# Kernel optimization log

Measured on AMD Instinct MI355X. Metric: run time of the kernel, lower is better.

## Reference

```python
import jax, jax.numpy as jnp
import numpy as np

HIDDEN_DIM = 4096
NUM_EXPERTS = 64
THRESHOLD = 0.8


def setup_inputs() -> dict:
    key = jax.random.key(0)
    kx, kw = jax.random.split(key)
    x = jax.random.normal(kx, (4, 4096, HIDDEN_DIM), dtype=jnp.float32)
    # gate weight init: normal(0, 0.1), bias zeros (as in nn.init calls)
    W = jax.random.normal(kw, (HIDDEN_DIM, NUM_EXPERTS), dtype=jnp.float32) * 0.1
    b = jnp.zeros((NUM_EXPERTS,), dtype=jnp.float32)
    return {"x": x, "W": W, "b": b}


def reference(x, W, b):
    # logits: [B, S, E]
    logits = jnp.einsum('bsh,he->bse', x, W) + b
    probs = jax.nn.softmax(logits, axis=-1)
    # descending sort over experts
    order = jnp.argsort(-probs, axis=-1)                        # [B,S,E] int
    sorted_probs = jnp.take_along_axis(probs, order, axis=-1)   # [B,S,E]
    cum = jnp.cumsum(sorted_probs, axis=-1)
    mask = cum >= THRESHOLD                                     # [B,S,E] bool
    k_values = jnp.argmax(mask.astype(jnp.float32), axis=-1) + 1
    never = ~jnp.any(mask, axis=-1)
    k_values = jnp.where(never, NUM_EXPERTS, k_values)          # [B,S] int
    # Vectorized mask-and-scatter replacing the per-token Python loop.
    # Padded to NUM_EXPERTS (static max_k) for jit compatibility; slots
    # beyond k get expert=-1, prob=0 exactly as the torch fill defaults.
    slot = jnp.arange(NUM_EXPERTS)                              # [E]
    sel = slot[None, None, :] < k_values[..., None]             # [B,S,E]
    selected_experts = jnp.where(sel, order, -1)
    selected_probs = jnp.where(sel, sorted_probs, 0.0)
    return selected_experts, selected_probs, k_values
```

## Files before the change

kernel.cpp:

```cpp
#include <hip/hip_runtime.h>
#include <math.h>

#define HID 4096
#define NEXP 64
#define NTOK 16384

typedef __attribute__((ext_vector_type(8))) short short8;
typedef __attribute__((ext_vector_type(8))) __bf16 bf16x8;
typedef __attribute__((ext_vector_type(4))) float f32x4;

__global__ __launch_bounds__(256) void wfrag_kernel(
    const float* __restrict__ W, short* __restrict__ wfh,
    short* __restrict__ wfl, unsigned int* __restrict__ flag_count) {
  if (blockIdx.x == 0 && threadIdx.x == 0) *flag_count = 0u;
  int gid = blockIdx.x * 256 + threadIdx.x;
  int l  = gid & 63;
  int nt = (gid >> 6) & 3;
  int ks = gid >> 8;
  int e  = nt * 16 + (l & 15);
  int k0 = ks * 32 + (l >> 4) * 8;
  bf16x8 h8, l8;
#pragma unroll
  for (int j = 0; j < 8; ++j) {
    float w = W[(size_t)(k0 + j) * NEXP + e];
    __bf16 h = (__bf16)w;
    h8[j] = h;
    l8[j] = (__bf16)(w - (float)h);
  }
  ((short8*)wfh)[gid] = __builtin_bit_cast(short8, h8);
  ((short8*)wfl)[gid] = __builtin_bit_cast(short8, l8);
}

template <int P>
__device__ __forceinline__ void issue_b(const short8*& wh, const short8*& wl,
                                        short8 (&rbh)[2][4],
                                        short8 (&rbl)[2][4]) {
#pragma unroll
  for (int nt = 0; nt < 4; ++nt) {
    rbh[P][nt] = wh[nt * 64];
    rbl[P][nt] = wl[nt * 64];
  }
  wh += 256;
  wl += 256;
}

template <int P>
__device__ __forceinline__ void issue_g(const float* (&xp)[4][2],
                                        float* wavebase ) {
#pragma unroll
  for (int st = 0; st < 4; ++st)
#pragma unroll
    for (int p = 0; p < 2; ++p)
      __builtin_amdgcn_global_load_lds(xp[st][p],
                                       wavebase + P * 2048 + st * 512 + p * 256,
                                       16, 0, 0);
#pragma unroll
  for (int st = 0; st < 4; ++st) {
    xp[st][0] += 32;
    xp[st][1] += 32;
  }
}

template <int P>
__device__ __forceinline__ void compute_c(const float* wavebase,
                                          short8 (&rbh)[2][4],
                                          short8 (&rbl)[2][4],
                                          f32x4 (&acc)[4][4], int l) {
  const int lr = l >> 4;
  const int s0 = ((2 * lr) ^ (l & 7)) * 16;
  const char* cb = (const char*)(wavebase + P * 2048);
#pragma unroll
  for (int st = 0; st < 4; ++st) {
    const char* rowbase =
        cb + st * 2048 + ((l >> 3) & 1) * 1024 + (l & 7) * 128;
    float4 lo = *(const float4*)(rowbase + s0);
    float4 hi = *(const float4*)(rowbase + (s0 ^ 16));
    float xv[8] = {lo.x, lo.y, lo.z, lo.w, hi.x, hi.y, hi.z, hi.w};
    bf16x8 ah, al;
#pragma unroll
    for (int j = 0; j < 8; ++j) {
      __bf16 h = (__bf16)xv[j];
      ah[j] = h;
      al[j] = (__bf16)(xv[j] - (float)h);
    }
#pragma unroll
    for (int nt = 0; nt < 4; ++nt) {
      bf16x8 vh = __builtin_bit_cast(bf16x8, rbh[P][nt]);
      bf16x8 vl = __builtin_bit_cast(bf16x8, rbl[P][nt]);
      acc[st][nt] = __builtin_amdgcn_mfma_f32_16x16x32_bf16(ah, vh, acc[st][nt], 0, 0, 0);
      acc[st][nt] = __builtin_amdgcn_mfma_f32_16x16x32_bf16(al, vh, acc[st][nt], 0, 0, 0);
      acc[st][nt] = __builtin_amdgcn_mfma_f32_16x16x32_bf16(ah, vl, acc[st][nt], 0, 0, 0);
      acc[st][nt] = __builtin_amdgcn_mfma_f32_16x16x32_bf16(al, vl, acc[st][nt], 0, 0, 0);
    }
  }
}

#define SB __builtin_amdgcn_sched_barrier(0)
#define WAIT16 asm volatile("s_waitcnt vmcnt(16)" ::: "memory")
#define WAIT0  asm volatile("s_waitcnt vmcnt(0)" ::: "memory")

__global__ __launch_bounds__(512, 2) void gemm_kernel(
    const float* __restrict__ x, const short* __restrict__ wfh,
    const short* __restrict__ wfl, float* __restrict__ partial) {
  __shared__ float smem[32768];

  const int t = threadIdx.x;
  const int w = t >> 6;
  const int l = t & 63;
  const int lr = l >> 4;
  const int m0 = blockIdx.x * 64;
  const int kq = w * (HID / 8);

  float* wavebase = smem + w * 4096;

  const float* xp[4][2];
#pragma unroll
  for (int st = 0; st < 4; ++st)
#pragma unroll
    for (int p = 0; p < 2; ++p) {
      int g = (l & 7) ^ (l >> 3);
      int row = m0 + st * 16 + 8 * p + (l >> 3);
      xp[st][p] = x + (size_t)row * HID + kq + g * 4;
    }

  const short8* wh = (const short8*)wfh + (size_t)(w * 16 * 4) * 64 + l;
  const short8* wl = (const short8*)wfl + (size_t)(w * 16 * 4) * 64 + l;

  f32x4 acc[4][4];
#pragma unroll
  for (int st = 0; st < 4; ++st)
#pragma unroll
    for (int nt = 0; nt < 4; ++nt) acc[st][nt] = (f32x4){0.f, 0.f, 0.f, 0.f};

  short8 rbh[2][4], rbl[2][4];

  issue_b<0>(wh, wl, rbh, rbl);
  SB;
  issue_g<0>(xp, wavebase);
  SB;

#pragma unroll 1
  for (int c2 = 0; c2 < 7; ++c2) {
    issue_b<1>(wh, wl, rbh, rbl);
    SB;
    issue_g<1>(xp, wavebase);
    SB;
    WAIT16;
    SB;
    compute_c<0>(wavebase, rbh, rbl, acc, l);

    issue_b<0>(wh, wl, rbh, rbl);
    SB;
    issue_g<0>(xp, wavebase);
    SB;
    WAIT16;
    SB;
    compute_c<1>(wavebase, rbh, rbl, acc, l);
  }
  issue_b<1>(wh, wl, rbh, rbl);
  SB;
  issue_g<1>(xp, wavebase);
  SB;
  WAIT16;
  SB;
  compute_c<0>(wavebase, rbh, rbl, acc, l);
  WAIT0;
  SB;
  compute_c<1>(wavebase, rbh, rbl, acc, l);

  __syncthreads();
  float* red = smem;
  if (w >= 4) {
#pragma unroll
    for (int st = 0; st < 4; ++st)
#pragma unroll
      for (int nt = 0; nt < 4; ++nt)
#pragma unroll
        for (int r = 0; r < 4; ++r)
          red[((w - 4) * 64 + st * 16 + lr * 4 + r) * 68 + nt * 16 +
              (l & 15)] = acc[st][nt][r];
  }
  __syncthreads();
  if (w < 4) {
#pragma unroll
    for (int st = 0; st < 4; ++st)
#pragma unroll
      for (int nt = 0; nt < 4; ++nt)
#pragma unroll
        for (int r = 0; r < 4; ++r) {
          int row = st * 16 + lr * 4 + r;
          float s = acc[st][nt][r] +
                    red[(w * 64 + row) * 68 + nt * 16 + (l & 15)];
          partial[((size_t)w * NTOK + m0 + row) * NEXP + nt * 16 + (l & 15)] =
              s;
        }
  }
}

__global__ __launch_bounds__(256) void route_kernel(
    const float* __restrict__ partial, const float* __restrict__ b,
    float* __restrict__ out_exp, float* __restrict__ out_prob,
    float* __restrict__ out_k, unsigned int* __restrict__ flag_count,
    int* __restrict__ flag_list) {
  const int tok = (int)((blockIdx.x * 256 + threadIdx.x) >> 6);
  const int l   = threadIdx.x & 63;

  float p0 = partial[((size_t)0 * NTOK + tok) * NEXP + l];
  float p1 = partial[((size_t)1 * NTOK + tok) * NEXP + l];
  float p2 = partial[((size_t)2 * NTOK + tok) * NEXP + l];
  float p3 = partial[((size_t)3 * NTOK + tok) * NEXP + l];
  float lgv = (p0 + p1) + (p2 + p3) + b[l];

  float mx = lgv;
#pragma unroll
  for (int off = 32; off; off >>= 1) mx = fmaxf(mx, __shfl_xor(mx, off));
  float ev = expf(lgv - mx);
  float sm = ev;
#pragma unroll
  for (int off = 32; off; off >>= 1) sm += __shfl_xor(sm, off);
  float p = ev / sm;

  float sp = p;
  int   si = l;
#pragma unroll
  for (int k = 2; k <= 64; k <<= 1) {
#pragma unroll
    for (int j = k >> 1; j > 0; j >>= 1) {
      float op = __shfl_xor(sp, j);
      int   oi = __shfl_xor(si, j);
      bool cmp  = (sp > op) || (sp == op && si < oi);
      bool keep = (cmp == (((l & k) == 0) == ((l & j) == 0)));
      if (!keep) { sp = op; si = oi; }
    }
  }

  float c = sp;
#pragma unroll
  for (int off = 1; off < 64; off <<= 1) {
    float tp = __shfl_up(c, off);
    if (l >= off) c += tp;
  }

  unsigned long long m = __ballot(c >= 0.8f);
  int kv = (m == 0ULL) ? NEXP : __ffsll(m);

  float spn = __shfl_down(sp, 1);
  bool pairRisk = (l < kv) && (l < 63) && ((sp - spn) < 1e-3f * (sp + spn));
  bool cumRisk  = fabsf(c - 0.8f) < 3e-4f;
  bool flagged  = (__ballot(pairRisk || cumRisk) != 0ULL);

  bool sel = l < kv;
  size_t base = (size_t)tok * NEXP;
  out_exp[base + l]  = sel ? (float)si : -1.0f;
  out_prob[base + l] = sel ? sp : 0.0f;
  if (l == 0) {
    out_k[tok] = (float)kv;
    if (flagged) {
      unsigned int idx = atomicAdd(flag_count, 1u);
      flag_list[idx] = tok;
    }
  }
}

__global__ __launch_bounds__(256) void router_repair(
    const float* __restrict__ x, const float* __restrict__ W,
    const float* __restrict__ b, const unsigned int* __restrict__ flag_count,
    const int* __restrict__ flag_list, float* __restrict__ out_exp,
    float* __restrict__ out_prob, float* __restrict__ out_k) {
  __shared__ double part[4][NEXP];
  const int t = threadIdx.x;
  const int e = t & 63;
  const int c = t >> 6;
  const int n = (int)*flag_count;

  for (int i = blockIdx.x; i < n; i += gridDim.x) {
    const int tok = flag_list[i];
    const float* xrow = x + (size_t)tok * HID;
    double s = 0.0;
    const int k0 = c * (HID / 4);
#pragma unroll 8
    for (int k = k0; k < k0 + HID / 4; ++k)
      s = fma((double)xrow[k], (double)W[(size_t)k * NEXP + e], s);
    part[c][e] = s;
    __syncthreads();

    if (t < 64) {
      double lgv = ((part[0][e] + part[1][e]) + part[2][e]) + part[3][e] +
                   (double)b[e];
      double mx = lgv;
#pragma unroll
      for (int off = 32; off; off >>= 1) mx = fmax(mx, __shfl_xor(mx, off));
      double ev = exp(lgv - mx);
      double sm = ev;
#pragma unroll
      for (int off = 32; off; off >>= 1) sm += __shfl_xor(sm, off);
      double p = ev / sm;

      double sp = p;
      int    si = e;
#pragma unroll
      for (int k = 2; k <= 64; k <<= 1) {
#pragma unroll
        for (int j = k >> 1; j > 0; j >>= 1) {
          double op = __shfl_xor(sp, j);
          int    oi = __shfl_xor(si, j);
          bool cmp  = (sp > op) || (sp == op && si < oi);
          bool keep = (cmp == (((e & k) == 0) == ((e & j) == 0)));
          if (!keep) { sp = op; si = oi; }
        }
      }

      double cc = sp;
#pragma unroll
      for (int off = 1; off < 64; off <<= 1) {
        double tp = __shfl_up(cc, off);
        if (e >= off) cc += tp;
      }

      unsigned long long m = __ballot(cc >= 0.8);
      int kv = (m == 0ULL) ? NEXP : __ffsll(m);

      bool sel = e < kv;
      size_t base = (size_t)tok * NEXP;
      out_exp[base + e]  = sel ? (float)si : -1.0f;
      out_prob[base + e] = sel ? (float)sp : 0.0f;
      if (e == 0) out_k[tok] = (float)kv;
    }
    __syncthreads();
  }
}

extern "C" void kernel_launch(void* const* d_in, const int* in_sizes, int n_in,
                              void* d_out, int out_size, void* d_ws,
                              size_t ws_size, hipStream_t stream) {
  const float* x = (const float*)d_in[0];
  const float* W = (const float*)d_in[1];
  const float* b = (const float*)d_in[2];

  float* out_exp  = (float*)d_out;
  float* out_prob = out_exp + (size_t)NTOK * NEXP;
  float* out_k    = out_prob + (size_t)NTOK * NEXP;

  short* wfh = (short*)d_ws;
  short* wfl = (short*)((char*)d_ws + (size_t)512 * 1024);
  unsigned int* flag_count = (unsigned int*)((char*)d_ws + (size_t)1024 * 1024);
  int* flag_list = (int*)((char*)d_ws + (size_t)1024 * 1024 + 256);
  float* partial = (float*)((char*)d_ws + (size_t)2 * 1024 * 1024);

  wfrag_kernel<<<128, 256, 0, stream>>>(W, wfh, wfl, flag_count);
  gemm_kernel<<<NTOK / 64, 512, 0, stream>>>(x, wfh, wfl, partial);
  route_kernel<<<NTOK * NEXP / 256, 256, 0, stream>>>(
      partial, b, out_exp, out_prob, out_k, flag_count, flag_list);
  router_repair<<<128, 256, 0, stream>>>(x, W, b, flag_count, flag_list,
                                         out_exp, out_prob, out_k);
}
```

Baseline: 117.4 us.

## Shrink GEMM token tile to 32 and write 8 split-K partial planes

The GEMM block now covers 32 tokens instead of 64 with smaller accumulators and a 2-stage LDS buffer, which allows 4 blocks per CU and doubles the grid. The in-block LDS reduction across wave pairs is removed, so each of 8 waves writes its own K-slice partial plane and the route kernel sums 8 planes instead of 4. This trades higher occupancy and less sync for twice as much partial-buffer traffic and twice as many W fragment reloads per token.

```diff
diff --git a/kernel.cpp b/kernel.cpp
--- a/kernel.cpp
+++ b/kernel.cpp
@@ -4,6 +4,7 @@
 #define HID 4096
 #define NEXP 64
 #define NTOK 16384
+#define NPLANE 8
 
 typedef __attribute__((ext_vector_type(8))) short short8;
 typedef __attribute__((ext_vector_type(8))) __bf16 bf16x8;
@@ -31,91 +32,25 @@
   ((short8*)wfl)[gid] = __builtin_bit_cast(short8, l8);
 }
 
-template <int P>
-__device__ __forceinline__ void issue_b(const short8*& wh, const short8*& wl,
-                                        short8 (&rbh)[2][4],
-                                        short8 (&rbl)[2][4]) {
-#pragma unroll
-  for (int nt = 0; nt < 4; ++nt) {
-    rbh[P][nt] = wh[nt * 64];
-    rbl[P][nt] = wl[nt * 64];
-  }
-  wh += 256;
-  wl += 256;
-}
-
-template <int P>
-__device__ __forceinline__ void issue_g(const float* (&xp)[4][2],
-                                        float* wavebase ) {
-#pragma unroll
-  for (int st = 0; st < 4; ++st)
-#pragma unroll
-    for (int p = 0; p < 2; ++p)
-      __builtin_amdgcn_global_load_lds(xp[st][p],
-                                       wavebase + P * 2048 + st * 512 + p * 256,
-                                       16, 0, 0);
-#pragma unroll
-  for (int st = 0; st < 4; ++st) {
-    xp[st][0] += 32;
-    xp[st][1] += 32;
-  }
-}
-
-template <int P>
-__device__ __forceinline__ void compute_c(const float* wavebase,
-                                          short8 (&rbh)[2][4],
-                                          short8 (&rbl)[2][4],
-                                          f32x4 (&acc)[4][4], int l) {
-  const int lr = l >> 4;
-  const int s0 = ((2 * lr) ^ (l & 7)) * 16;
-  const char* cb = (const char*)(wavebase + P * 2048);
-#pragma unroll
-  for (int st = 0; st < 4; ++st) {
-    const char* rowbase =
-        cb + st * 2048 + ((l >> 3) & 1) * 1024 + (l & 7) * 128;
-    float4 lo = *(const float4*)(rowbase + s0);
-    float4 hi = *(const float4*)(rowbase + (s0 ^ 16));
-    float xv[8] = {lo.x, lo.y, lo.z, lo.w, hi.x, hi.y, hi.z, hi.w};
-    bf16x8 ah, al;
-#pragma unroll
-    for (int j = 0; j < 8; ++j) {
-      __bf16 h = (__bf16)xv[j];
-      ah[j] = h;
-      al[j] = (__bf16)(xv[j] - (float)h);
-    }
-#pragma unroll
-    for (int nt = 0; nt < 4; ++nt) {
-      bf16x8 vh = __builtin_bit_cast(bf16x8, rbh[P][nt]);
-      bf16x8 vl = __builtin_bit_cast(bf16x8, rbl[P][nt]);
-      acc[st][nt] = __builtin_amdgcn_mfma_f32_16x16x32_bf16(ah, vh, acc[st][nt], 0, 0, 0);
-      acc[st][nt] = __builtin_amdgcn_mfma_f32_16x16x32_bf16(al, vh, acc[st][nt], 0, 0, 0);
-      acc[st][nt] = __builtin_amdgcn_mfma_f32_16x16x32_bf16(ah, vl, acc[st][nt], 0, 0, 0);
-      acc[st][nt] = __builtin_amdgcn_mfma_f32_16x16x32_bf16(al, vl, acc[st][nt], 0, 0, 0);
-    }
-  }
-}
-
 #define SB __builtin_amdgcn_sched_barrier(0)
-#define WAIT16 asm volatile("s_waitcnt vmcnt(16)" ::: "memory")
-#define WAIT0  asm volatile("s_waitcnt vmcnt(0)" ::: "memory")
-
-__global__ __launch_bounds__(512, 2) void gemm_kernel(
+#define WAIT4 asm volatile("s_waitcnt vmcnt(4)" ::: "memory")
+#define WAIT0 asm volatile("s_waitcnt vmcnt(0)" ::: "memory")
+
+__global__ __launch_bounds__(512, 4) void gemm_kernel(
     const float* __restrict__ x, const short* __restrict__ wfh,
     const short* __restrict__ wfl, float* __restrict__ partial) {
-  __shared__ float smem[32768];
+  __shared__ float xstage[8][2][1024];
 
   const int t = threadIdx.x;
   const int w = t >> 6;
   const int l = t & 63;
   const int lr = l >> 4;
-  const int m0 = blockIdx.x * 64;
+  const int m0 = blockIdx.x * 32;
   const int kq = w * (HID / 8);
 
-  float* wavebase = smem + w * 4096;
-
-  const float* xp[4][2];
-#pragma unroll
-  for (int st = 0; st < 4; ++st)
+  const float* xp[2][2];
+#pragma unroll
+  for (int st = 0; st < 2; ++st)
 #pragma unroll
     for (int p = 0; p < 2; ++p) {
       int g = (l & 7) ^ (l >> 3);
@@ -123,78 +58,103 @@
       xp[st][p] = x + (size_t)row * HID + kq + g * 4;
     }
 
-  const short8* wh = (const short8*)wfh + (size_t)(w * 16 * 4) * 64 + l;
-  const short8* wl = (const short8*)wfl + (size_t)(w * 16 * 4) * 64 + l;
-
-  f32x4 acc[4][4];
-#pragma unroll
-  for (int st = 0; st < 4; ++st)
+  const short8* wh = (const short8*)wfh + (size_t)(w * 16) * 256 + l;
+  const short8* wl = (const short8*)wfl + (size_t)(w * 16) * 256 + l;
+
+  f32x4 acc[2][4];
+#pragma unroll
+  for (int st = 0; st < 2; ++st)
 #pragma unroll
     for (int nt = 0; nt < 4; ++nt) acc[st][nt] = (f32x4){0.f, 0.f, 0.f, 0.f};
 
-  short8 rbh[2][4], rbl[2][4];
-
-  issue_b<0>(wh, wl, rbh, rbl);
+  short8 rbh[4], rbl[4];
+
+#pragma unroll
+  for (int st = 0; st < 2; ++st)
+#pragma unroll
+    for (int p = 0; p < 2; ++p)
+      __builtin_amdgcn_global_load_lds(xp[st][p],
+                                       &xstage[w][0][st * 512 + p * 256], 16,
+                                       0, 0);
   SB;
-  issue_g<0>(xp, wavebase);
+#pragma unroll
+  for (int nt = 0; nt < 4; ++nt) {
+    rbh[nt] = wh[nt * 64];
+    rbl[nt] = wl[nt * 64];
+  }
+  wh += 256;
+  wl += 256;
   SB;
 
 #pragma unroll 1
-  for (int c2 = 0; c2 < 7; ++c2) {
-    issue_b<1>(wh, wl, rbh, rbl);
+  for (int ch = 0; ch < 16; ++ch) {
+    const int cur = ch & 1;
+    if (ch < 15) {
+      const int nxt = cur ^ 1;
+#pragma unroll
+      for (int st = 0; st < 2; ++st)
+#pragma unroll
+        for (int p = 0; p < 2; ++p)
+          __builtin_amdgcn_global_load_lds(
+              xp[st][p] + (ch + 1) * 32,
+              &xstage[w][nxt][st * 512 + p * 256], 16, 0, 0);
+      SB;
+      WAIT4;
+    } else {
+      WAIT0;
+    }
     SB;
-    issue_g<1>(xp, wavebase);
+
+    {
+      const char* cb = (const char*)&xstage[w][cur][0];
+      const int s0 = ((2 * lr) ^ (l & 7)) * 16;
+#pragma unroll
+      for (int st = 0; st < 2; ++st) {
+        const char* rowbase =
+            cb + st * 2048 + ((l >> 3) & 1) * 1024 + (l & 7) * 128;
+        float4 lo = *(const float4*)(rowbase + s0);
+        float4 hi = *(const float4*)(rowbase + (s0 ^ 16));
+        float xv[8] = {lo.x, lo.y, lo.z, lo.w, hi.x, hi.y, hi.z, hi.w};
+        bf16x8 ah, al;
+#pragma unroll
+        for (int j = 0; j < 8; ++j) {
+          __bf16 h = (__bf16)xv[j];
+          ah[j] = h;
+          al[j] = (__bf16)(xv[j] - (float)h);
+        }
+#pragma unroll
+        for (int nt = 0; nt < 4; ++nt) {
+          bf16x8 vh = __builtin_bit_cast(bf16x8, rbh[nt]);
+          bf16x8 vl = __builtin_bit_cast(bf16x8, rbl[nt]);
+          acc[st][nt] = __builtin_amdgcn_mfma_f32_16x16x32_bf16(ah, vh, acc[st][nt], 0, 0, 0);
+          acc[st][nt] = __builtin_amdgcn_mfma_f32_16x16x32_bf16(al, vh, acc[st][nt], 0, 0, 0);
+          acc[st][nt] = __builtin_amdgcn_mfma_f32_16x16x32_bf16(ah, vl, acc[st][nt], 0, 0, 0);
+          acc[st][nt] = __builtin_amdgcn_mfma_f32_16x16x32_bf16(al, vl, acc[st][nt], 0, 0, 0);
+        }
+      }
+    }
     SB;
-    WAIT16;
+
+    if (ch < 15) {
+#pragma unroll
+      for (int nt = 0; nt < 4; ++nt) {
+        rbh[nt] = wh[nt * 64];
+        rbl[nt] = wl[nt * 64];
+      }
+      wh += 256;
+      wl += 256;
+    }
     SB;
-    compute_c<0>(wavebase, rbh, rbl, acc, l);
-
-    issue_b<0>(wh, wl, rbh, rbl);
-    SB;
-    issue_g<0>(xp, wavebase);
-    SB;
-    WAIT16;
-    SB;
-    compute_c<1>(wavebase, rbh, rbl, acc, l);
-  }
-  issue_b<1>(wh, wl, rbh, rbl);
-  SB;
-  issue_g<1>(xp, wavebase);
-  SB;
-  WAIT16;
-  SB;
-  compute_c<0>(wavebase, rbh, rbl, acc, l);
-  WAIT0;
-  SB;
-  compute_c<1>(wavebase, rbh, rbl, acc, l);
-
-  __syncthreads();
-  float* red = smem;
-  if (w >= 4) {
-#pragma unroll
-    for (int st = 0; st < 4; ++st)
-#pragma unroll
-      for (int nt = 0; nt < 4; ++nt)
-#pragma unroll
-        for (int r = 0; r < 4; ++r)
-          red[((w - 4) * 64 + st * 16 + lr * 4 + r) * 68 + nt * 16 +
-              (l & 15)] = acc[st][nt][r];
-  }
-  __syncthreads();
-  if (w < 4) {
-#pragma unroll
-    for (int st = 0; st < 4; ++st)
-#pragma unroll
-      for (int nt = 0; nt < 4; ++nt)
-#pragma unroll
-        for (int r = 0; r < 4; ++r) {
-          int row = st * 16 + lr * 4 + r;
-          float s = acc[st][nt][r] +
-                    red[(w * 64 + row) * 68 + nt * 16 + (l & 15)];
-          partial[((size_t)w * NTOK + m0 + row) * NEXP + nt * 16 + (l & 15)] =
-              s;
-        }
-  }
+  }
+
+#pragma unroll
+  for (int st = 0; st < 2; ++st)
+#pragma unroll
+    for (int nt = 0; nt < 4; ++nt)
+#pragma unroll
+      for (int r = 0; r < 4; ++r)
+        partial[((size_t)w * NTOK + m0 + st * 16 + lr * 4 + r) * NEXP +
+                nt * 16 + (l & 15)] = acc[st][nt][r];
 }
 
 __global__ __launch_bounds__(256) void route_kernel(
@@ -205,11 +165,12 @@
   const int tok = (int)((blockIdx.x * 256 + threadIdx.x) >> 6);
   const int l   = threadIdx.x & 63;
 
-  float p0 = partial[((size_t)0 * NTOK + tok) * NEXP + l];
-  float p1 = partial[((size_t)1 * NTOK + tok) * NEXP + l];
-  float p2 = partial[((size_t)2 * NTOK + tok) * NEXP + l];
-  float p3 = partial[((size_t)3 * NTOK + tok) * NEXP + l];
-  float lgv = (p0 + p1) + (p2 + p3) + b[l];
+  float p[NPLANE];
+#pragma unroll
+  for (int j = 0; j < NPLANE; ++j)
+    p[j] = partial[((size_t)j * NTOK + tok) * NEXP + l];
+  float lgv = (((p[0] + p[1]) + (p[2] + p[3])) +
+               ((p[4] + p[5]) + (p[6] + p[7]))) + b[l];
 
   float mx = lgv;
 #pragma unroll
@@ -218,9 +179,9 @@
   float sm = ev;
 #pragma unroll
   for (int off = 32; off; off >>= 1) sm += __shfl_xor(sm, off);
-  float p = ev / sm;
-
-  float sp = p;
+  float pr = ev / sm;
+
+  float sp = pr;
   int   si = l;
 #pragma unroll
   for (int k = 2; k <= 64; k <<= 1) {
@@ -348,7 +309,7 @@
   float* partial = (float*)((char*)d_ws + (size_t)2 * 1024 * 1024);
 
   wfrag_kernel<<<128, 256, 0, stream>>>(W, wfh, wfl, flag_count);
-  gemm_kernel<<<NTOK / 64, 512, 0, stream>>>(x, wfh, wfl, partial);
+  gemm_kernel<<<NTOK / 32, 512, 0, stream>>>(x, wfh, wfl, partial);
   route_kernel<<<NTOK * NEXP / 256, 256, 0, stream>>>(
       partial, b, out_exp, out_prob, out_k, flag_count, flag_list);
   router_repair<<<128, 256, 0, stream>>>(x, W, b, flag_count, flag_list,
```

After: 136.5 us. 1.16x slower.

## Fuse routing (softmax, sort, threshold) into GEMM epilogue via shared memory

Applied to the files above, without the earlier changes.

Merges the separate route kernel into the GEMM epilogue. All eight waves write their K-split partial accumulators to shared memory (odd stride to avoid bank conflicts), then each wave reduces and routes eight tokens. This removes the global partial-logits buffer round trip (4 x 16384 x 64 floats written and read back) and one kernel launch. The cost is a larger shared-memory footprint (about 130 KB per block), which may limit two blocks per CU. The routing epilogue is also now serialized inside the GEMM blocks.

```diff
diff --git a/kernel.cpp b/kernel.cpp
--- a/kernel.cpp
+++ b/kernel.cpp
@@ -4,6 +4,7 @@
 #define HID 4096
 #define NEXP 64
 #define NTOK 16384
+#define PSTR 65
 
 typedef __attribute__((ext_vector_type(8))) short short8;
 typedef __attribute__((ext_vector_type(8))) __bf16 bf16x8;
@@ -99,10 +100,13 @@
 #define WAIT16 asm volatile("s_waitcnt vmcnt(16)" ::: "memory")
 #define WAIT0  asm volatile("s_waitcnt vmcnt(0)" ::: "memory")
 
-__global__ __launch_bounds__(512, 2) void gemm_kernel(
+__global__ __launch_bounds__(512, 2) void gemm_route_kernel(
     const float* __restrict__ x, const short* __restrict__ wfh,
-    const short* __restrict__ wfl, float* __restrict__ partial) {
-  __shared__ float smem[32768];
+    const short* __restrict__ wfl, const float* __restrict__ b,
+    float* __restrict__ out_exp, float* __restrict__ out_prob,
+    float* __restrict__ out_k, unsigned int* __restrict__ flag_count,
+    int* __restrict__ flag_list) {
+  __shared__ float smem[8 * 64 * PSTR];
 
   const int t = threadIdx.x;
   const int w = t >> 6;
@@ -123,8 +127,8 @@
       xp[st][p] = x + (size_t)row * HID + kq + g * 4;
     }
 
-  const short8* wh = (const short8*)wfh + (size_t)(w * 16 * 4) * 64 + l;
-  const short8* wl = (const short8*)wfl + (size_t)(w * 16 * 4) * 64 + l;
+  const short8* wh = (const short8*)wfh + (size_t)(w * 16) * 256 + l;
+  const short8* wl = (const short8*)wfl + (size_t)(w * 16) * 256 + l;
 
   f32x4 acc[4][4];
 #pragma unroll
@@ -169,95 +173,79 @@
   compute_c<1>(wavebase, rbh, rbl, acc, l);
 
   __syncthreads();
-  float* red = smem;
-  if (w >= 4) {
-#pragma unroll
-    for (int st = 0; st < 4; ++st)
-#pragma unroll
-      for (int nt = 0; nt < 4; ++nt)
-#pragma unroll
-        for (int r = 0; r < 4; ++r)
-          red[((w - 4) * 64 + st * 16 + lr * 4 + r) * 68 + nt * 16 +
-              (l & 15)] = acc[st][nt][r];
-  }
+  float* part = smem;
+#pragma unroll
+  for (int st = 0; st < 4; ++st)
+#pragma unroll
+    for (int nt = 0; nt < 4; ++nt)
+#pragma unroll
+      for (int r = 0; r < 4; ++r)
+        part[(w * 64 + st * 16 + lr * 4 + r) * PSTR + nt * 16 + (l & 15)] =
+            acc[st][nt][r];
   __syncthreads();
-  if (w < 4) {
-#pragma unroll
-    for (int st = 0; st < 4; ++st)
-#pragma unroll
-      for (int nt = 0; nt < 4; ++nt)
-#pragma unroll
-        for (int r = 0; r < 4; ++r) {
-          int row = st * 16 + lr * 4 + r;
-          float s = acc[st][nt][r] +
-                    red[(w * 64 + row) * 68 + nt * 16 + (l & 15)];
-          partial[((size_t)w * NTOK + m0 + row) * NEXP + nt * 16 + (l & 15)] =
-              s;
-        }
-  }
-}
-
-__global__ __launch_bounds__(256) void route_kernel(
-    const float* __restrict__ partial, const float* __restrict__ b,
-    float* __restrict__ out_exp, float* __restrict__ out_prob,
-    float* __restrict__ out_k, unsigned int* __restrict__ flag_count,
-    int* __restrict__ flag_list) {
-  const int tok = (int)((blockIdx.x * 256 + threadIdx.x) >> 6);
-  const int l   = threadIdx.x & 63;
-
-  float p0 = partial[((size_t)0 * NTOK + tok) * NEXP + l];
-  float p1 = partial[((size_t)1 * NTOK + tok) * NEXP + l];
-  float p2 = partial[((size_t)2 * NTOK + tok) * NEXP + l];
-  float p3 = partial[((size_t)3 * NTOK + tok) * NEXP + l];
-  float lgv = (p0 + p1) + (p2 + p3) + b[l];
-
-  float mx = lgv;
-#pragma unroll
-  for (int off = 32; off; off >>= 1) mx = fmaxf(mx, __shfl_xor(mx, off));
-  float ev = expf(lgv - mx);
-  float sm = ev;
-#pragma unroll
-  for (int off = 32; off; off >>= 1) sm += __shfl_xor(sm, off);
-  float p = ev / sm;
-
-  float sp = p;
-  int   si = l;
-#pragma unroll
-  for (int k = 2; k <= 64; k <<= 1) {
-#pragma unroll
-    for (int j = k >> 1; j > 0; j >>= 1) {
-      float op = __shfl_xor(sp, j);
-      int   oi = __shfl_xor(si, j);
-      bool cmp  = (sp > op) || (sp == op && si < oi);
-      bool keep = (cmp == (((l & k) == 0) == ((l & j) == 0)));
-      if (!keep) { sp = op; si = oi; }
-    }
-  }
-
-  float c = sp;
-#pragma unroll
-  for (int off = 1; off < 64; off <<= 1) {
-    float tp = __shfl_up(c, off);
-    if (l >= off) c += tp;
-  }
-
-  unsigned long long m = __ballot(c >= 0.8f);
-  int kv = (m == 0ULL) ? NEXP : __ffsll(m);
-
-  float spn = __shfl_down(sp, 1);
-  bool pairRisk = (l < kv) && (l < 63) && ((sp - spn) < 1e-3f * (sp + spn));
-  bool cumRisk  = fabsf(c - 0.8f) < 3e-4f;
-  bool flagged  = (__ballot(pairRisk || cumRisk) != 0ULL);
-
-  bool sel = l < kv;
-  size_t base = (size_t)tok * NEXP;
-  out_exp[base + l]  = sel ? (float)si : -1.0f;
-  out_prob[base + l] = sel ? sp : 0.0f;
-  if (l == 0) {
-    out_k[tok] = (float)kv;
-    if (flagged) {
-      unsigned int idx = atomicAdd(flag_count, 1u);
-      flag_list[idx] = tok;
+
+  const float bias = b[l];
+  for (int it = 0; it < 8; ++it) {
+    const int tl = w * 8 + it;
+    float a0 = part[(0 * 64 + tl) * PSTR + l];
+    float a1 = part[(1 * 64 + tl) * PSTR + l];
+    float a2 = part[(2 * 64 + tl) * PSTR + l];
+    float a3 = part[(3 * 64 + tl) * PSTR + l];
+    float a4 = part[(4 * 64 + tl) * PSTR + l];
+    float a5 = part[(5 * 64 + tl) * PSTR + l];
+    float a6 = part[(6 * 64 + tl) * PSTR + l];
+    float a7 = part[(7 * 64 + tl) * PSTR + l];
+    float lgv = ((a0 + a1) + (a2 + a3)) + ((a4 + a5) + (a6 + a7)) + bias;
+
+    float mx = lgv;
+#pragma unroll
+    for (int off = 32; off; off >>= 1) mx = fmaxf(mx, __shfl_xor(mx, off));
+    float ev = expf(lgv - mx);
+    float sm = ev;
+#pragma unroll
+    for (int off = 32; off; off >>= 1) sm += __shfl_xor(sm, off);
+    float pr = ev / sm;
+
+    float sp = pr;
+    int   si = l;
+#pragma unroll
+    for (int k = 2; k <= 64; k <<= 1) {
+#pragma unroll
+      for (int j = k >> 1; j > 0; j >>= 1) {
+        float op = __shfl_xor(sp, j);
+        int   oi = __shfl_xor(si, j);
+        bool cmp  = (sp > op) || (sp == op && si < oi);
+        bool keep = (cmp == (((l & k) == 0) == ((l & j) == 0)));
+        if (!keep) { sp = op; si = oi; }
+      }
+    }
+
+    float c = sp;
+#pragma unroll
+    for (int off = 1; off < 64; off <<= 1) {
+      float tp = __shfl_up(c, off);
+      if (l >= off) c += tp;
+    }
+
+    unsigned long long m = __ballot(c >= 0.8f);
+    int kv = (m == 0ULL) ? NEXP : __ffsll(m);
+
+    float spn = __shfl_down(sp, 1);
+    bool pairRisk = (l < kv) && (l < 63) && ((sp - spn) < 1e-3f * (sp + spn));
+    bool cumRisk  = fabsf(c - 0.8f) < 3e-4f;
+    bool flagged  = (__ballot(pairRisk || cumRisk) != 0ULL);
+
+    bool sel = l < kv;
+    const int tok = m0 + tl;
+    size_t base = (size_t)tok * NEXP;
+    out_exp[base + l]  = sel ? (float)si : -1.0f;
+    out_prob[base + l] = sel ? sp : 0.0f;
+    if (l == 0) {
+      out_k[tok] = (float)kv;
+      if (flagged) {
+        unsigned int idx = atomicAdd(flag_count, 1u);
+        flag_list[idx] = tok;
+      }
     }
   }
 }
@@ -345,12 +333,10 @@
   short* wfl = (short*)((char*)d_ws + (size_t)512 * 1024);
   unsigned int* flag_count = (unsigned int*)((char*)d_ws + (size_t)1024 * 1024);
   int* flag_list = (int*)((char*)d_ws + (size_t)1024 * 1024 + 256);
-  float* partial = (float*)((char*)d_ws + (size_t)2 * 1024 * 1024);
 
   wfrag_kernel<<<128, 256, 0, stream>>>(W, wfh, wfl, flag_count);
-  gemm_kernel<<<NTOK / 64, 512, 0, stream>>>(x, wfh, wfl, partial);
-  route_kernel<<<NTOK * NEXP / 256, 256, 0, stream>>>(
-      partial, b, out_exp, out_prob, out_k, flag_count, flag_list);
+  gemm_route_kernel<<<NTOK / 64, 512, 0, stream>>>(
+      x, wfh, wfl, b, out_exp, out_prob, out_k, flag_count, flag_list);
   router_repair<<<128, 256, 0, stream>>>(x, W, b, flag_count, flag_list,
                                          out_exp, out_prob, out_k);
 }
```

Result: no change. 117.6 us (+0.2%).
